# Kernel tuning notes

Hardware: AMD Instinct MI355X
Metric: run time of the kernel (lower is better)

Reference implementation:

```python
import jax, jax.numpy as jnp
import numpy as np
from jax import lax

EPS = 1e-5

def _conv3x3(x, w):
    # x: [N,C,H,W], w: [O,I,3,3]
    return lax.conv_general_dilated(x, w, window_strides=(1, 1),
                                    padding=((1, 1), (1, 1)),
                                    dimension_numbers=('NCHW', 'OIHW', 'NCHW'))

def _bn(x, gamma, beta, mean, var):
    # inference-mode batchnorm, per-channel over dim 1
    scale = (gamma * lax.rsqrt(var + EPS))[None, :, None, None]
    shift = (beta - mean * gamma * lax.rsqrt(var + EPS))[None, :, None, None]
    return x * scale + shift

def setup_inputs() -> dict:
    key = jax.random.key(0)
    ks = jax.random.split(key, 11)
    N, C, H, W = 64, 128, 56, 56
    d = {}
    d['x'] = jax.random.normal(ks[0], (N, C, H, W), dtype=jnp.float32)
    d['w1'] = jax.random.normal(ks[1], (C, C, 3, 3), dtype=jnp.float32) * (1.0 / np.sqrt(9 * C))
    d['g1'] = jax.random.uniform(ks[2], (C,), dtype=jnp.float32, minval=0.5, maxval=1.5)
    d['b1'] = jax.random.normal(ks[3], (C,), dtype=jnp.float32) * 0.1
    d['m1'] = jax.random.normal(ks[4], (C,), dtype=jnp.float32) * 0.1
    d['v1'] = jax.random.uniform(ks[5], (C,), dtype=jnp.float32, minval=0.5, maxval=1.5)
    d['w2'] = jax.random.normal(ks[6], (C, C, 3, 3), dtype=jnp.float32) * (1.0 / np.sqrt(9 * C))
    d['g2'] = jax.random.uniform(ks[7], (C,), dtype=jnp.float32, minval=0.5, maxval=1.5)
    d['b2'] = jax.random.normal(ks[8], (C,), dtype=jnp.float32) * 0.1
    d['m2'] = jax.random.normal(ks[9], (C,), dtype=jnp.float32) * 0.1
    d['v2'] = jax.random.uniform(ks[10], (C,), dtype=jnp.float32, minval=0.5, maxval=1.5)
    return d

def reference(x, w1, g1, b1, m1, v1, w2, g2, b2, m2, v2):
    identity = x  # downsample is None (stride=1, inplanes==planes)
    out = _conv3x3(x, w1)
    out = jax.nn.relu(_bn(out, g1, b1, m1, v1))
    out = _conv3x3(out, w2)
    out = _bn(out, g2, b2, m2, v2)
    out = out + identity
    return jax.nn.relu(out)
```

## Files before the change

### kernel.cpp

```cpp
#include <hip/hip_runtime.h>
#include <hip/hip_bf16.h>

typedef __attribute__((ext_vector_type(8))) short short8;
typedef __attribute__((ext_vector_type(16))) float f32x16;
typedef __attribute__((ext_vector_type(4))) float f32x4;

static constexpr int NN = 64;
static constexpr int C  = 128;
static constexpr int H  = 56;
static constexpr int W  = 56;
static constexpr int HP = 58;
static constexpr int ROWB = HP * 256;
static constexpr int XSLOT = 15360;

__device__ __forceinline__ void gload16(const void* g, void* l) {
    __builtin_amdgcn_global_load_lds(
        (const __attribute__((address_space(1))) unsigned int*)g,
        (__attribute__((address_space(3))) unsigned int*)l, 16, 0, 0);
}

__device__ __forceinline__ f32x16 mfma32(short8 a, short8 b, f32x16 c) {
    return __builtin_amdgcn_mfma_f32_32x32x16_bf16(a, b, c, 0, 0, 0);
}

__global__ __launch_bounds__(128)
void pack_weights(const float* __restrict__ w, const float* __restrict__ g,
                  const float* __restrict__ b, const float* __restrict__ m,
                  const float* __restrict__ v, __hip_bfloat16* __restrict__ Wp2,
                  float* __restrict__ shift)
{
    int o = blockIdx.x;
    int c = threadIdx.x;
    float scale = g[o] * rsqrtf(v[o] + 1e-5f);
    if (c == 0) shift[o] = b[o] - m[o] * scale;
    const float* ws = w + ((size_t)o * C + c) * 9;
    int ks = c >> 4, hi = (c >> 3) & 1, j = c & 7;
    #pragma unroll
    for (int tap = 0; tap < 9; ++tap) {
        size_t idx = ((((size_t)tap * 8 + ks) * 2 + hi) * 128 + o) * 8 + j;
        Wp2[idx] = __float2bfloat16(ws[tap] * scale);
    }
}

__global__ __launch_bounds__(256)
void transform_x(const float* __restrict__ x, __hip_bfloat16* __restrict__ Xp)
{
    __shared__ float t[C * 57];
    int bid = blockIdx.x;
    int n = bid / H, h = bid % H;
    int tid = threadIdx.x;

    #pragma unroll
    for (int i = 0; i < 7; ++i) {
        int idx4 = i * 256 + tid;
        int c  = idx4 / 14;
        int wq = (idx4 % 14) * 4;
        const float* p = x + ((size_t)(n * C + c)) * (H * W) + h * W + wq;
        float4 vv = *(const float4*)p;
        t[c * 57 + wq + 0] = vv.x;
        t[c * 57 + wq + 1] = vv.y;
        t[c * 57 + wq + 2] = vv.z;
        t[c * 57 + wq + 3] = vv.w;
    }
    __syncthreads();
    #pragma unroll
    for (int i = 0; i < 28; ++i) {
        int idx = i * 256 + tid;
        int c = idx & 127, w = idx >> 7;
        float vv = t[c * 57 + w];
        Xp[(((size_t)n * HP + (h + 1)) * HP + (w + 1)) * C + c] = __float2bfloat16(vv);
    }
}

__global__ __launch_bounds__(256)
void zero_halo(__hip_bfloat16* __restrict__ buf)
{
    int idx = blockIdx.x * 256 + threadIdx.x;
    int n = idx / (228 * 16);
    int rem = idx % (228 * 16);
    int p = rem >> 4, l = rem & 15;
    int y, xq;
    if (p < 58)       { y = 0;  xq = p; }
    else if (p < 116) { y = 57; xq = p - 58; }
    else { int q = p - 116; y = 1 + (q >> 1); xq = (q & 1) * 57; }
    short8* dst = (short8*)(buf + (((size_t)n * HP + y) * HP + xq) * C + l * 8);
    *dst = short8{0,0,0,0,0,0,0,0};
}

template<int WHICH>
__global__ __launch_bounds__(256, 2)
void conv3x3_kernel(const __hip_bfloat16* __restrict__ Xp,
                    const __hip_bfloat16* __restrict__ Wp2,
                    const float* __restrict__ shift,
                    const float* __restrict__ ident,
                    void* __restrict__ outp)
{
    __shared__ char s_x[3 * XSLOT + 2304];
    __shared__ char s_w[2][16384];

    const int tid  = threadIdx.x;
    const int wave = tid >> 6;
    const int lane = tid & 63;
    const int lr5  = lane & 31;
    const int hi   = lane >> 5;
    const int wm   = wave >> 1;
    const int oh   = wave & 1;

    const int bid0 = blockIdx.x;
    const int bid  = (bid0 & 7) * 224 + (bid0 >> 3);
    const int n = bid / 28, h0 = (bid % 28) * 2;

    const char* xbase = (const char*)Xp + ((size_t)n * HP + h0) * ROWB;

    #pragma unroll
    for (int slot = 0; slot < 3; ++slot)
        #pragma unroll
        for (int i = 0; i < 4; ++i) {
            int blk = wave + i * 4;
            if (blk < 15) {
                int d = blk * 1024 + lane * 16;
                int s = d ^ (((d >> 8) & 15) << 4);
                gload16(xbase + (size_t)slot * ROWB + s, s_x + slot * XSLOT + d);
            }
        }
    #pragma unroll
    for (int i = 0; i < 4; ++i) {
        int d = (wave * 4 + i) * 1024 + lane * 16;
        int s = d ^ (((d >> 7) & 3) << 5);
        gload16((const char*)Wp2 + s, s_w[0] + d);
    }

    int wboff[2][4];
    #pragma unroll
    for (int of = 0; of < 2; ++of)
        #pragma unroll
        for (int ks = 0; ks < 4; ++ks) {
            int r = (ks * 2 + hi) * 2048 + (oh * 64 + of * 32 + lr5) * 16;
            wboff[of][ks] = r ^ (((r >> 7) & 3) << 5);
        }

    const int sb0 = ((0 + wm) % 3) * XSLOT;
    const int sb1 = ((1 + wm) % 3) * XSLOT;
    const int sb2 = ((2 + wm) % 3) * XSLOT;

    f32x16 acc[2][2];
    #pragma unroll
    for (int i = 0; i < 2; ++i)
        #pragma unroll
        for (int j = 0; j < 2; ++j)
            acc[i][j] = f32x16{0,0,0,0,0,0,0,0,0,0,0,0,0,0,0,0};

    #pragma unroll
    for (int ht = 0; ht < 18; ++ht) {
        __syncthreads();
        if (ht < 17) {
            const char* wsrc = (const char*)Wp2 + (size_t)(ht + 1) * 16384;
            #pragma unroll
            for (int i = 0; i < 4; ++i) {
                int d = (wave * 4 + i) * 1024 + lane * 16;
                int s = d ^ (((d >> 7) & 3) << 5);
                gload16(wsrc + s, s_w[(ht + 1) & 1] + d);
            }
        }
        if (ht == 6) {
            #pragma unroll
            for (int i = 0; i < 4; ++i) {
                int blk = wave + i * 4;
                if (blk < 15) {
                    int d = blk * 1024 + lane * 16;
                    int s = d ^ (((d >> 8) & 15) << 4);
                    gload16(xbase + (size_t)3 * ROWB + s, s_x + d);
                }
            }
        }
        const int tap = ht >> 1;
        const int kh = tap / 3, kw = tap % 3;
        const int sbase = (kh == 0) ? sb0 : (kh == 1 ? sb1 : sb2);
        const char* wcur = s_w[ht & 1];
        const int rowA = lr5 + kw;
        #pragma unroll
        for (int ks = 0; ks < 4; ++ks) {
            const int cb = ((ht & 1) * 4 + ks) * 32 + hi * 16;
            short8 xa0, xa1, wb0, wb1;
            {
                int off = (rowA * 256 + cb) ^ ((rowA & 15) << 4);
                xa0 = *(const short8*)(s_x + sbase + off);
            }
            {
                int row = rowA + 32;
                int off = (row * 256 + cb) ^ ((row & 15) << 4);
                xa1 = *(const short8*)(s_x + sbase + off);
            }
            wb0 = *(const short8*)(wcur + wboff[0][ks]);
            wb1 = *(const short8*)(wcur + wboff[1][ks]);
            if (WHICH == 0) {
                acc[0][0] = mfma32(xa0, wb0, acc[0][0]);
                acc[0][1] = mfma32(xa0, wb1, acc[0][1]);
                acc[1][0] = mfma32(xa1, wb0, acc[1][0]);
                acc[1][1] = mfma32(xa1, wb1, acc[1][1]);
            } else {
                acc[0][0] = mfma32(wb0, xa0, acc[0][0]);
                acc[0][1] = mfma32(wb0, xa1, acc[0][1]);
                acc[1][0] = mfma32(wb1, xa0, acc[1][0]);
                acc[1][1] = mfma32(wb1, xa1, acc[1][1]);
            }
        }
    }

    if (WHICH == 0) {
        __hip_bfloat16* o1 = (__hip_bfloat16*)outp;
        size_t rowb = ((size_t)n * HP + (h0 + wm + 1)) * HP;
        #pragma unroll
        for (int of = 0; of < 2; ++of) {
            int o = oh * 64 + of * 32 + lr5;
            float sh = shift[o];
            #pragma unroll
            for (int mf = 0; mf < 2; ++mf) {
                #pragma unroll
                for (int r = 0; r < 16; ++r) {
                    int m = mf * 32 + 4 * hi + (r & 3) + 8 * (r >> 2);
                    if (m < W) {
                        float f = acc[mf][of][r] + sh;
                        f = f > 0.f ? f : 0.f;
                        o1[(rowb + m + 1) * C + o] = __float2bfloat16(f);
                    }
                }
            }
        }
    } else {
        float* o2 = (float*)outp;
        int h = h0 + wm;
        #pragma unroll
        for (int mf = 0; mf < 2; ++mf) {
            int m = mf * 32 + lr5;
            if (m < W) {
                #pragma unroll
                for (int of = 0; of < 2; ++of) {
                    #pragma unroll
                    for (int q = 0; q < 4; ++q) {
                        int ob = oh * 64 + of * 32 + 4 * hi + 8 * q;
                        f32x4 sh = *(const f32x4*)(shift + ob);
                        #pragma unroll
                        for (int j = 0; j < 4; ++j) {
                            int o = ob + j;
                            size_t idx = ((size_t)(n * C + o) * H + h) * W + m;
                            float f = acc[of][mf][q * 4 + j] + sh[j] + ident[idx];
                            o2[idx] = f > 0.f ? f : 0.f;
                        }
                    }
                }
            }
        }
    }
}

extern "C" void kernel_launch(void* const* d_in, const int* in_sizes, int n_in,
                              void* d_out, int out_size, void* d_ws, size_t ws_size,
                              hipStream_t stream)
{
    const float* x  = (const float*)d_in[0];
    const float* w1 = (const float*)d_in[1];
    const float* g1 = (const float*)d_in[2];
    const float* b1 = (const float*)d_in[3];
    const float* m1 = (const float*)d_in[4];
    const float* v1 = (const float*)d_in[5];
    const float* w2 = (const float*)d_in[6];
    const float* g2 = (const float*)d_in[7];
    const float* b2 = (const float*)d_in[8];
    const float* m2 = (const float*)d_in[9];
    const float* v2 = (const float*)d_in[10];
    float* out = (float*)d_out;

    char* ws = (char*)d_ws;
    const size_t PADBUF = (size_t)NN * HP * HP * C * 2;
    const size_t WBUF   = (size_t)9 * 8 * 2 * 128 * 8 * 2;
    size_t oX  = 0;
    size_t oY  = oX + PADBUF + 32768;
    size_t oW1 = oY + PADBUF + 32768;
    size_t oW2 = oW1 + WBUF;
    size_t oS1 = oW2 + WBUF;
    size_t oS2 = oS1 + 512;

    __hip_bfloat16* Xp  = (__hip_bfloat16*)(ws + oX);
    __hip_bfloat16* Y1  = (__hip_bfloat16*)(ws + oY);
    __hip_bfloat16* W1p = (__hip_bfloat16*)(ws + oW1);
    __hip_bfloat16* W2p = (__hip_bfloat16*)(ws + oW2);
    float* s1 = (float*)(ws + oS1);
    float* s2 = (float*)(ws + oS2);

    zero_halo<<<912, 256, 0, stream>>>(Xp);
    zero_halo<<<912, 256, 0, stream>>>(Y1);

    pack_weights<<<128, 128, 0, stream>>>(w1, g1, b1, m1, v1, W1p, s1);
    pack_weights<<<128, 128, 0, stream>>>(w2, g2, b2, m2, v2, W2p, s2);
    transform_x<<<NN * H, 256, 0, stream>>>(x, Xp);

    conv3x3_kernel<0><<<NN * 28, 256, 0, stream>>>(Xp, W1p, s1, nullptr, (void*)Y1);
    conv3x3_kernel<1><<<NN * 28, 256, 0, stream>>>(Y1, W2p, s2, x, (void*)out);
}
```

Baseline: 281.4 us.

## Process four output rows per block and read weights directly from global

```diff
diff --git a/kernel.cpp b/kernel.cpp
--- a/kernel.cpp
+++ b/kernel.cpp
@@ -88,15 +88,14 @@
 }
 
 template<int WHICH>
-__global__ __launch_bounds__(256, 2)
+__global__ __launch_bounds__(512, 4)
 void conv3x3_kernel(const __hip_bfloat16* __restrict__ Xp,
                     const __hip_bfloat16* __restrict__ Wp2,
                     const float* __restrict__ shift,
                     const float* __restrict__ ident,
                     void* __restrict__ outp)
 {
-    __shared__ char s_x[3 * XSLOT + 2304];
-    __shared__ char s_w[2][16384];
+    __shared__ char s_x[5 * XSLOT + 2048];
 
     const int tid  = threadIdx.x;
     const int wave = tid >> 6;
@@ -107,41 +106,23 @@
     const int oh   = wave & 1;
 
     const int bid0 = blockIdx.x;
-    const int bid  = (bid0 & 7) * 224 + (bid0 >> 3);
-    const int n = bid / 28, h0 = (bid % 28) * 2;
+    const int bid  = (bid0 & 7) * 112 + (bid0 >> 3);
+    const int n = bid / 14, h0 = (bid % 14) * 4;
 
     const char* xbase = (const char*)Xp + ((size_t)n * HP + h0) * ROWB;
 
     #pragma unroll
-    for (int slot = 0; slot < 3; ++slot)
-        #pragma unroll
-        for (int i = 0; i < 4; ++i) {
-            int blk = wave + i * 4;
-            if (blk < 15) {
-                int d = blk * 1024 + lane * 16;
-                int s = d ^ (((d >> 8) & 15) << 4);
-                gload16(xbase + (size_t)slot * ROWB + s, s_x + slot * XSLOT + d);
-            }
-        }
-    #pragma unroll
-    for (int i = 0; i < 4; ++i) {
-        int d = (wave * 4 + i) * 1024 + lane * 16;
-        int s = d ^ (((d >> 7) & 3) << 5);
-        gload16((const char*)Wp2 + s, s_w[0] + d);
-    }
-
-    int wboff[2][4];
-    #pragma unroll
-    for (int of = 0; of < 2; ++of)
-        #pragma unroll
-        for (int ks = 0; ks < 4; ++ks) {
-            int r = (ks * 2 + hi) * 2048 + (oh * 64 + of * 32 + lr5) * 16;
-            wboff[of][ks] = r ^ (((r >> 7) & 3) << 5);
-        }
-
-    const int sb0 = ((0 + wm) % 3) * XSLOT;
-    const int sb1 = ((1 + wm) % 3) * XSLOT;
-    const int sb2 = ((2 + wm) % 3) * XSLOT;
+    for (int i = 0; i < 8; ++i) {
+        int u = wave + i * 8;
+        if (u < 60) {
+            int q = u / 15, blk = u % 15;
+            int d = blk * 1024 + lane * 16;
+            int s = d ^ (((d >> 8) & 15) << 4);
+            gload16(xbase + (size_t)q * ROWB + s, s_x + q * XSLOT + d);
+        }
+    }
+
+    const __hip_bfloat16* wlane = Wp2 + hi * 1024 + (oh * 64 + lr5) * 8;
 
     f32x16 acc[2][2];
     #pragma unroll
@@ -150,62 +131,66 @@
         for (int j = 0; j < 2; ++j)
             acc[i][j] = f32x16{0,0,0,0,0,0,0,0,0,0,0,0,0,0,0,0};
 
-    #pragma unroll
-    for (int ht = 0; ht < 18; ++ht) {
-        __syncthreads();
-        if (ht < 17) {
-            const char* wsrc = (const char*)Wp2 + (size_t)(ht + 1) * 16384;
-            #pragma unroll
-            for (int i = 0; i < 4; ++i) {
-                int d = (wave * 4 + i) * 1024 + lane * 16;
-                int s = d ^ (((d >> 7) & 3) << 5);
-                gload16(wsrc + s, s_w[(ht + 1) & 1] + d);
-            }
-        }
-        if (ht == 6) {
-            #pragma unroll
-            for (int i = 0; i < 4; ++i) {
-                int blk = wave + i * 4;
-                if (blk < 15) {
-                    int d = blk * 1024 + lane * 16;
-                    int s = d ^ (((d >> 8) & 15) << 4);
-                    gload16(xbase + (size_t)3 * ROWB + s, s_x + d);
-                }
-            }
-        }
-        const int tap = ht >> 1;
-        const int kh = tap / 3, kw = tap % 3;
-        const int sbase = (kh == 0) ? sb0 : (kh == 1 ? sb1 : sb2);
-        const char* wcur = s_w[ht & 1];
-        const int rowA = lr5 + kw;
-        #pragma unroll
-        for (int ks = 0; ks < 4; ++ks) {
-            const int cb = ((ht & 1) * 4 + ks) * 32 + hi * 16;
-            short8 xa0, xa1, wb0, wb1;
-            {
-                int off = (rowA * 256 + cb) ^ ((rowA & 15) << 4);
-                xa0 = *(const short8*)(s_x + sbase + off);
-            }
-            {
-                int row = rowA + 32;
-                int off = (row * 256 + cb) ^ ((row & 15) << 4);
-                xa1 = *(const short8*)(s_x + sbase + off);
-            }
-            wb0 = *(const short8*)(wcur + wboff[0][ks]);
-            wb1 = *(const short8*)(wcur + wboff[1][ks]);
-            if (WHICH == 0) {
-                acc[0][0] = mfma32(xa0, wb0, acc[0][0]);
-                acc[0][1] = mfma32(xa0, wb1, acc[0][1]);
-                acc[1][0] = mfma32(xa1, wb0, acc[1][0]);
-                acc[1][1] = mfma32(xa1, wb1, acc[1][1]);
-            } else {
-                acc[0][0] = mfma32(wb0, xa0, acc[0][0]);
-                acc[0][1] = mfma32(wb0, xa1, acc[0][1]);
-                acc[1][0] = mfma32(wb1, xa0, acc[1][0]);
-                acc[1][1] = mfma32(wb1, xa1, acc[1][1]);
-            }
-        }
-    }
+#define KHBLOCK(KH)                                                          \
+    _Pragma("unroll")                                                        \
+    for (int t = 0; t < 6; ++t) {                                            \
+        const int ht = (KH) * 6 + t;                                         \
+        const int tap = ht >> 1;                                             \
+        const int kw = tap % 3;                                              \
+        const int sbase = (((KH) + wm) % 5) * XSLOT;                         \
+        const int rowA = lr5 + kw;                                           \
+        _Pragma("unroll")                                                    \
+        for (int ks = 0; ks < 4; ++ks) {                                     \
+            const int ksg = (ht & 1) * 4 + ks;                               \
+            const int cb = ksg * 32 + hi * 16;                               \
+            short8 wb0 = *(const short8*)(wlane + (ht * 4 + ks) * 2048);     \
+            short8 wb1 = *(const short8*)(wlane + (ht * 4 + ks) * 2048 + 256); \
+            int off0 = (rowA * 256 + cb) ^ ((rowA & 15) << 4);               \
+            short8 xa0 = *(const short8*)(s_x + sbase + off0);               \
+            int row1 = rowA + 32;                                            \
+            int off1 = (row1 * 256 + cb) ^ ((row1 & 15) << 4);               \
+            short8 xa1 = *(const short8*)(s_x + sbase + off1);               \
+            if (WHICH == 0) {                      \
+                acc[0][0] = mfma32(xa0, wb0, acc[0][0]);                     \
+                acc[0][1] = mfma32(xa0, wb1, acc[0][1]);                     \
+                acc[1][0] = mfma32(xa1, wb0, acc[1][0]);                     \
+                acc[1][1] = mfma32(xa1, wb1, acc[1][1]);                     \
+            } else {                               \
+                acc[0][0] = mfma32(wb0, xa0, acc[0][0]);                     \
+                acc[0][1] = mfma32(wb0, xa1, acc[0][1]);                     \
+                acc[1][0] = mfma32(wb1, xa0, acc[1][0]);                     \
+                acc[1][1] = mfma32(wb1, xa1, acc[1][1]);                     \
+            }                                                                \
+        }                                                                    \
+    }
+
+    __syncthreads();
+    {
+        int d = wave * 1024 + lane * 16;
+        int s = d ^ (((d >> 8) & 15) << 4);
+        gload16(xbase + (size_t)4 * ROWB + s, s_x + 4 * XSLOT + d);
+        if (wave < 7) {
+            int d2 = (wave + 8) * 1024 + lane * 16;
+            int s2 = d2 ^ (((d2 >> 8) & 15) << 4);
+            gload16(xbase + (size_t)4 * ROWB + s2, s_x + 4 * XSLOT + d2);
+        }
+    }
+    KHBLOCK(0)
+    __syncthreads();
+    {
+        int d = wave * 1024 + lane * 16;
+        int s = d ^ (((d >> 8) & 15) << 4);
+        gload16(xbase + (size_t)5 * ROWB + s, s_x + d);
+        if (wave < 7) {
+            int d2 = (wave + 8) * 1024 + lane * 16;
+            int s2 = d2 ^ (((d2 >> 8) & 15) << 4);
+            gload16(xbase + (size_t)5 * ROWB + s2, s_x + d2);
+        }
+    }
+    KHBLOCK(1)
+    __syncthreads();
+    KHBLOCK(2)
+#undef KHBLOCK
 
     if (WHICH == 0) {
         __hip_bfloat16* o1 = (__hip_bfloat16*)outp;
@@ -295,6 +280,6 @@
     pack_weights<<<128, 128, 0, stream>>>(w2, g2, b2, m2, v2, W2p, s2);
     transform_x<<<NN * H, 256, 0, stream>>>(x, Xp);
 
-    conv3x3_kernel<0><<<NN * 28, 256, 0, stream>>>(Xp, W1p, s1, nullptr, (void*)Y1);
-    conv3x3_kernel<1><<<NN * 28, 256, 0, stream>>>(Y1, W2p, s2, x, (void*)out);
-}
+    conv3x3_kernel<0><<<NN * 14, 512, 0, stream>>>(Xp, W1p, s1, nullptr, (void*)Y1);
+    conv3x3_kernel<1><<<NN * 14, 512, 0, stream>>>(Y1, W2p, s2, x, (void*)out);
+}
```

After: 368.6 us. 31.0% more time.
